# Performance work log

Hardware: AMD Instinct MI355X
Metric: run time of the kernel (lower is better)

The kernel has to match this reference:

```python
import jax, jax.numpy as jnp
import numpy as np

SIGMA = 1.0  # GaussianKernel slope


def setup_inputs() -> dict:
    key = jax.random.key(0)
    ks = jax.random.split(key, 6)
    B, F, E = 2048, 65536, 128
    return {
        "rel": jax.random.normal(ks[0], (B, E), dtype=jnp.float32),
        "arg1": jax.random.normal(ks[1], (B, E), dtype=jnp.float32),
        "arg2": jax.random.normal(ks[2], (B, E), dtype=jnp.float32),
        "fact_rel": jax.random.normal(ks[3], (F, E), dtype=jnp.float32),
        "fact_arg1": jax.random.normal(ks[4], (F, E), dtype=jnp.float32),
        "fact_arg2": jax.random.normal(ks[5], (F, E), dtype=jnp.float32),
    }


def reference(rel, arg1, arg2, fact_rel, fact_arg1, fact_arg2):
    # query: [B, 3E], facts: [F, 3E]  (concat scoring)
    query = jnp.concatenate([rel, arg1, arg2], axis=1)
    facts = jnp.concatenate([fact_rel, fact_arg1, fact_arg2], axis=1)
    # Gaussian kernel: exp(-||q - f||^2 / (2*sigma^2)), via ||q||^2 - 2 q.f + ||f||^2
    q_sq = jnp.sum(query * query, axis=1, keepdims=True)          # [B, 1]
    f_sq = jnp.sum(facts * facts, axis=1)                          # [F]
    d2 = q_sq - 2.0 * jnp.einsum('bd,fd->bf', query, facts) + f_sq[None, :]
    d2 = jnp.maximum(d2, 0.0)  # numerical guard for squared distance
    scores = jnp.exp(-d2 / (2.0 * SIGMA * SIGMA))                  # [B, F]
    return jnp.max(scores, axis=1)                                 # [B]
```

## Files before the change

kernel.cpp:

```cpp
#include <hip/hip_runtime.h>


typedef __attribute__((ext_vector_type(4))) float f32x4;
typedef __attribute__((ext_vector_type(2))) long lx2;
typedef __attribute__((ext_vector_type(4))) long lx4;
typedef __attribute__((ext_vector_type(8))) int i32x8;
typedef __attribute__((ext_vector_type(8))) __bf16 bf16x8;
typedef __attribute__((ext_vector_type(4))) unsigned short us4;

#define AS1 __attribute__((address_space(1)))
#define AS3 __attribute__((address_space(3)))
__device__ __forceinline__ void gl2lds16(const void* g, void* l) {
    __builtin_amdgcn_global_load_lds((const AS1 unsigned int*)g,
                                     (AS3 unsigned int*)l, 16, 0, 0);
}

__device__ __forceinline__ unsigned char f2e4m3(float x) {
    unsigned int u = __float_as_uint(x);
    unsigned int sign = (u >> 24) & 0x80u;
    unsigned int a = u & 0x7fffffffu;
    if (a >= 0x43e00000u) return (unsigned char)(sign | 0x7e);
    if (a < 0x3c800000u) {
        int m = (int)rintf(__uint_as_float(a) * 512.0f);
        return (unsigned char)(sign | (unsigned)m);
    }
    unsigned int base = a - 0x3c000000u;
    unsigned int lsb = (base >> 20) & 1u;
    unsigned int code = (base + 0x7ffffu + lsb) >> 20;
    return (unsigned char)(sign | code);
}

__device__ __forceinline__ unsigned short f2bf(float f) {
    unsigned int u = __float_as_uint(f);
    u = (u + 0x7fffu + ((u >> 16) & 1u)) >> 16;
    return (unsigned short)u;
}

__device__ __forceinline__ void conv_row_fp8(const float* __restrict__ p0,
                                             const float* __restrict__ p1,
                                             const float* __restrict__ p2,
                                             int row, unsigned char* __restrict__ outb,
                                             float* __restrict__ sq) {
    const int lane = threadIdx.x & 63;
    float s = 0.f;
    if (lane < 48) {
        const int p = lane >> 4;
        const int off = (lane & 15) * 8;
        const float* src = ((p == 0) ? p0 : (p == 1) ? p1 : p2) + (size_t)row * 128 + off;
        const float4 v0 = *(const float4*)(src);
        const float4 v1 = *(const float4*)(src + 4);
        s = v0.x * v0.x + v0.y * v0.y + v0.z * v0.z + v0.w * v0.w +
            v1.x * v1.x + v1.y * v1.y + v1.z * v1.z + v1.w * v1.w;
        const int k = p * 128 + off;
        const int g = k >> 6;
        const int ss = (k >> 5) & 1;
        const int quad = (k >> 3) & 3;
        const int cs = quad ^ ((row >> 1) & 3);
        unsigned long long pk =
            (unsigned long long)f2e4m3(v0.x)        | ((unsigned long long)f2e4m3(v0.y) << 8) |
            ((unsigned long long)f2e4m3(v0.z) << 16) | ((unsigned long long)f2e4m3(v0.w) << 24) |
            ((unsigned long long)f2e4m3(v1.x) << 32) | ((unsigned long long)f2e4m3(v1.y) << 40) |
            ((unsigned long long)f2e4m3(v1.z) << 48) | ((unsigned long long)f2e4m3(v1.w) << 56);
        *(unsigned long long*)(outb + (size_t)row * 384 + g * 64 + cs * 16 + ss * 8) = pk;
    }
#pragma unroll
    for (int off = 32; off >= 1; off >>= 1) s += __shfl_xor(s, off, 64);
    if (lane == 0) sq[row] = s;
}

__global__ void prep_kernel(const float* __restrict__ rel, const float* __restrict__ a1,
                            const float* __restrict__ a2, const float* __restrict__ fr,
                            const float* __restrict__ fa1, const float* __restrict__ fa2,
                            unsigned char* __restrict__ Qf, unsigned char* __restrict__ Ff,
                            float* __restrict__ qsq, float* __restrict__ fsq,
                            unsigned int* __restrict__ outbits, int B, int F) {
    const int wave = (int)(threadIdx.x >> 6);
    const int nq = B / 4;
    if ((int)blockIdx.x < nq) {
        conv_row_fp8(rel, a1, a2, blockIdx.x * 4 + wave, Qf, qsq);
        if (blockIdx.x == 0)
            for (int i = threadIdx.x; i < B; i += 256) outbits[i] = 0x7f800000u;
    } else {
        const int row = ((int)blockIdx.x - nq) * 4 + wave;
        if (row < F) conv_row_fp8(fr, fa1, fa2, row, Ff, fsq);
    }
}

__device__ __forceinline__ void stage_tile(const unsigned char* __restrict__ Ff,
                                           unsigned char* buf, int n0, int tid) {
#pragma unroll
    for (int it = 0; it < 6; ++it) {
        int iid = it * 256 + tid;
        gl2lds16(Ff + (size_t)(n0 + ((iid >> 2) & 63)) * 384 +
                     (iid >> 9) * 128 + ((iid >> 8) & 1) * 64 + (iid & 3) * 16,
                 buf + (size_t)iid * 16);
    }
}

__global__ __launch_bounds__(256, 2)
void gemm_pipe_kernel(const unsigned char* __restrict__ Qf,
                      const unsigned char* __restrict__ Ff,
                      const float* __restrict__ qsq, const float* __restrict__ fsq,
                      unsigned int* __restrict__ outbits, int ntiles) {
    __shared__ __align__(16) unsigned char Bs[2][24576];

    const int tid = threadIdx.x;
    const int lane = tid & 63;
    const int wid = tid >> 6;
    const int col = lane & 15, quad = lane >> 4;
    const int swc = ((col >> 1) & 3);
    const int cp = (quad ^ swc) * 16;
    const int m0 = blockIdx.y * 256;
    const int nbase = blockIdx.x * (ntiles * 64);
    const int SCL = 0x7f;

    union pk_t { lx4 l; i32x8 i; };

    i32x8 af8[4][3];
#pragma unroll
    for (int i = 0; i < 4; ++i) {
        const unsigned char* base = Qf + (size_t)(m0 + wid * 64 + i * 16 + col) * 384;
#pragma unroll
        for (int kk = 0; kk < 3; ++kk) {
            lx2 t0 = *(const lx2*)(base + kk * 128 + cp);
            lx2 t1 = *(const lx2*)(base + kk * 128 + 64 + cp);
            pk_t p; p.l.x = t0.x; p.l.y = t0.y; p.l.z = t1.x; p.l.w = t1.y;
            af8[i][kk] = p.i;
        }
    }

    float rowmin[16];
#pragma unroll
    for (int v = 0; v < 16; ++v) rowmin[v] = 3.0e38f;

    float fs_cur[4], fs_nxt[4];
#pragma unroll
    for (int j = 0; j < 4; ++j) fs_cur[j] = fsq[nbase + j * 16 + col];

    stage_tile(Ff, Bs[0], nbase, tid);
    for (int t = 0; t < ntiles; ++t) {
        __syncthreads();
        if (t + 1 < ntiles) {
            stage_tile(Ff, Bs[(t + 1) & 1], nbase + (t + 1) * 64, tid);
#pragma unroll
            for (int j = 0; j < 4; ++j)
                fs_nxt[j] = fsq[nbase + (t + 1) * 64 + j * 16 + col];
        }
        const unsigned char* bb = Bs[t & 1];

        f32x4 acc[4][4];
#pragma unroll
        for (int j = 0; j < 4; ++j) {
            float seed = -0.5f * fs_cur[j];
            f32x4 z = {seed, seed, seed, seed};
#pragma unroll
            for (int i = 0; i < 4; ++i) acc[i][j] = z;
        }

        i32x8 bv[3];
#define LOADB(S, DST)                                                          \
        {                                                                      \
            const int _j = (S) / 3, _kk = (S) % 3;                             \
            const unsigned char* pb = bb + _kk * 8192 + (_j * 16 + col) * 64 + cp; \
            lx2 t0 = *(const lx2*)(pb);                                        \
            lx2 t1 = *(const lx2*)(pb + 4096);                                 \
            pk_t p; p.l.x = t0.x; p.l.y = t0.y; p.l.z = t1.x; p.l.w = t1.y;    \
            DST = p.i;                                                         \
        }
#define MFMAS(S, SRC)                                                          \
        {                                                                      \
            const int _j = (S) / 3, _kk = (S) % 3;                             \
            _Pragma("unroll") for (int _i = 0; _i < 4; ++_i)                   \
                acc[_i][_j] = __builtin_amdgcn_mfma_scale_f32_16x16x128_f8f6f4(\
                    af8[_i][_kk], SRC, acc[_i][_j], 0, 0, 0, SCL, 0, SCL);     \
        }
        LOADB(0, bv[0]);
        LOADB(1, bv[1]);
#pragma unroll
        for (int s = 0; s < 12; ++s) {
            if (s + 2 < 12) LOADB(s + 2, bv[(s + 2) % 3]);
            MFMAS(s, bv[s % 3]);
        }
#undef LOADB
#undef MFMAS

#pragma unroll
        for (int i = 0; i < 4; ++i)
#pragma unroll
            for (int r = 0; r < 4; ++r) {
                float mn = rowmin[i * 4 + r];
#pragma unroll
                for (int j = 0; j < 4; ++j)
                    mn = fminf(mn, -2.0f * acc[i][j][r]);
                rowmin[i * 4 + r] = mn;
            }
#pragma unroll
        for (int j = 0; j < 4; ++j) fs_cur[j] = fs_nxt[j];
    }

#pragma unroll
    for (int v = 0; v < 16; ++v) {
        float mn = rowmin[v];
#pragma unroll
        for (int off = 1; off < 16; off <<= 1) mn = fminf(mn, __shfl_xor(mn, off, 64));
        rowmin[v] = mn;
    }
    if (col == 0) {
#pragma unroll
        for (int i = 0; i < 4; ++i)
#pragma unroll
            for (int r = 0; r < 4; ++r) {
                const int row = m0 + wid * 64 + i * 16 + quad * 4 + r;
                float d2 = fmaxf(qsq[row] + rowmin[i * 4 + r], 0.0f);
                atomicMin(outbits + row, __float_as_uint(d2));
            }
    }
}

__global__ void finalize_kernel(float* out, int n) {
    int i = blockIdx.x * blockDim.x + threadIdx.x;
    if (i < n) {
        float d2 = __uint_as_float(((unsigned int*)out)[i]);
        out[i] = expf(-0.5f * d2);
    }
}

__global__ void init_min_kernel(unsigned int* ob, int n) {
    int i = blockIdx.x * blockDim.x + threadIdx.x;
    if (i < n) ob[i] = 0x7f800000u;
}

__global__ void conv_rows_kernel(const float* __restrict__ p0, const float* __restrict__ p1,
                                 const float* __restrict__ p2, unsigned short* __restrict__ outb,
                                 float* __restrict__ sq, int nrows) {
    const int lane = threadIdx.x & 63;
    const int wave = threadIdx.x >> 6;
    const int row = blockIdx.x * 4 + wave;
    if (row >= nrows) return;
    float s = 0.f;
#pragma unroll
    for (int c = 0; c < 6; ++c) {
        int k = c * 64 + lane;
        const float* src = (k < 128) ? p0 : (k < 256) ? p1 : p2;
        float v = src[(size_t)row * 128 + (k & 127)];
        s += v * v;
        if (outb) outb[(size_t)row * 384 + k] = f2bf(v);
    }
#pragma unroll
    for (int off = 32; off >= 1; off >>= 1) s += __shfl_xor(s, off, 64);
    if (lane == 0) sq[row] = s;
}

__global__ __launch_bounds__(256)
void gemm_lean_kernel(const unsigned short* __restrict__ Qb,
                      const float* __restrict__ f0, const float* __restrict__ f1,
                      const float* __restrict__ f2,
                      const float* __restrict__ qsq, const float* __restrict__ fsq,
                      unsigned int* __restrict__ outbits, int K) {
    __shared__ __align__(16) unsigned short As[128 * 32];
    __shared__ __align__(16) unsigned short Bs[128 * 32];
    __shared__ float smin[128 * 2];

    const int tid = threadIdx.x;
    const int lane = tid & 63;
    const int wid = tid >> 6;
    const int wm = wid >> 1, wn = wid & 1;
    const int col = lane & 15, quad = lane >> 4;
    const int m0 = blockIdx.x * 128;
    const int n0 = blockIdx.y * 128;

    f32x4 acc[4][4];
#pragma unroll
    for (int i = 0; i < 4; ++i)
#pragma unroll
        for (int j = 0; j < 4; ++j) {
            f32x4 z = {0.f, 0.f, 0.f, 0.f};
            acc[i][j] = z;
        }

    const int nk = K >> 5;
    for (int kk = 0; kk < nk; ++kk) {
        const int k0 = kk << 5;
        __syncthreads();
#pragma unroll
        for (int it = 0; it < 2; ++it) {
            int iid = it * 256 + tid;
            int row = iid >> 2, ch = iid & 3;
            gl2lds16(Qb + ((size_t)(m0 + row) * K + k0 + ch * 8), As + (row * 32 + ch * 8));
        }
        const float* src = (k0 < 128) ? f0 : (k0 < 256) ? f1 : f2;
        const int kp = k0 & 127;
#pragma unroll
        for (int it = 0; it < 4; ++it) {
            int iid = it * 256 + tid;
            int row = iid >> 3, ch = iid & 7;
            const float4 v = *(const float4*)(src + (size_t)(n0 + row) * 128 + kp + ch * 4);
            us4 w = {f2bf(v.x), f2bf(v.y), f2bf(v.z), f2bf(v.w)};
            *(us4*)(Bs + (row * 32 + ch * 4)) = w;
        }
        __syncthreads();

        bf16x8 afr[4], bfv[4];
#pragma unroll
        for (int i = 0; i < 4; ++i)
            afr[i] = *(const bf16x8*)(As + ((wm * 64 + i * 16 + col) * 32 + quad * 8));
#pragma unroll
        for (int j = 0; j < 4; ++j)
            bfv[j] = *(const bf16x8*)(Bs + ((wn * 64 + j * 16 + col) * 32 + quad * 8));
#pragma unroll
        for (int i = 0; i < 4; ++i)
#pragma unroll
            for (int j = 0; j < 4; ++j)
                acc[i][j] = __builtin_amdgcn_mfma_f32_16x16x32_bf16(afr[i], bfv[j], acc[i][j], 0, 0, 0);
    }

    float fs[4];
#pragma unroll
    for (int j = 0; j < 4; ++j) fs[j] = fsq[n0 + wn * 64 + j * 16 + col];
#pragma unroll
    for (int i = 0; i < 4; ++i) {
#pragma unroll
        for (int r = 0; r < 4; ++r) {
            const int mrow = wm * 64 + i * 16 + quad * 4 + r;
            const float qs = qsq[m0 + mrow];
            float mn = 3.0e38f;
#pragma unroll
            for (int j = 0; j < 4; ++j) {
                float d2 = qs + fs[j] - 2.0f * acc[i][j][r];
                mn = fminf(mn, fmaxf(d2, 0.0f));
            }
#pragma unroll
            for (int off = 1; off < 16; off <<= 1) mn = fminf(mn, __shfl_xor(mn, off, 64));
            if (col == 0) smin[mrow * 2 + wn] = mn;
        }
    }
    __syncthreads();
    if (tid < 128) {
        float v = fminf(smin[tid * 2 + 0], smin[tid * 2 + 1]);
        atomicMin(outbits + m0 + tid, __float_as_uint(v));
    }
}

__global__ __launch_bounds__(256)
void tier3_kernel(const float* __restrict__ rel, const float* __restrict__ a1,
                  const float* __restrict__ a2, const float* __restrict__ fr,
                  const float* __restrict__ fa1, const float* __restrict__ fa2,
                  unsigned int* __restrict__ outbits) {
    __shared__ float qs[16][384];
    __shared__ float red[4][16];
    const int tid = threadIdx.x;
    const int qbase = blockIdx.y * 16;
    const int fbase = blockIdx.x * 2048;
    for (int i = tid; i < 16 * 384; i += 256) {
        int r = i / 384, c = i % 384;
        const float* src = (c < 128) ? rel : (c < 256) ? a1 : a2;
        qs[r][c] = src[(size_t)(qbase + r) * 128 + (c & 127)];
    }
    __syncthreads();
    float mn[16];
#pragma unroll
    for (int q = 0; q < 16; ++q) mn[q] = 3.0e38f;
    for (int fi = 0; fi < 2048; fi += 256) {
        const int f = fbase + fi + tid;
        float acc[16];
#pragma unroll
        for (int q = 0; q < 16; ++q) acc[q] = 0.f;
#pragma unroll
        for (int p = 0; p < 3; ++p) {
            const float* fptr = ((p == 0) ? fr : (p == 1) ? fa1 : fa2) + (size_t)f * 128;
            for (int k4 = 0; k4 < 32; ++k4) {
                const float4 fv = *(const float4*)(fptr + k4 * 4);
#pragma unroll
                for (int q = 0; q < 16; ++q) {
                    float d0 = fv.x - qs[q][p * 128 + k4 * 4 + 0];
                    float d1 = fv.y - qs[q][p * 128 + k4 * 4 + 1];
                    float d2 = fv.z - qs[q][p * 128 + k4 * 4 + 2];
                    float d3 = fv.w - qs[q][p * 128 + k4 * 4 + 3];
                    acc[q] += d0 * d0 + d1 * d1 + d2 * d2 + d3 * d3;
                }
            }
        }
#pragma unroll
        for (int q = 0; q < 16; ++q) mn[q] = fminf(mn[q], fmaxf(acc[q], 0.f));
    }
#pragma unroll
    for (int q = 0; q < 16; ++q) {
        float v = mn[q];
#pragma unroll
        for (int off = 32; off >= 1; off >>= 1) v = fminf(v, __shfl_xor(v, off, 64));
        if ((tid & 63) == 0) red[tid >> 6][q] = v;
    }
    __syncthreads();
    if (tid < 16) {
        float v = fminf(fminf(red[0][tid], red[1][tid]), fminf(red[2][tid], red[3][tid]));
        atomicMin(outbits + qbase + tid, __float_as_uint(v));
    }
}

extern "C" void kernel_launch(void* const* d_in, const int* in_sizes, int n_in,
                              void* d_out, int out_size, void* d_ws, size_t ws_size,
                              hipStream_t stream) {
    const float* rel = (const float*)d_in[0];
    const float* a1 = (const float*)d_in[1];
    const float* a2 = (const float*)d_in[2];
    const float* fr = (const float*)d_in[3];
    const float* fa1 = (const float*)d_in[4];
    const float* fa2 = (const float*)d_in[5];

    const int E = 128, K = 384;
    const int B = in_sizes[0] / E;
    const int F = in_sizes[3] / E;

    float* out = (float*)d_out;
    unsigned int* outbits = (unsigned int*)d_out;

    const size_t ff_bytes = (size_t)F * K;
    const size_t qf_bytes = (size_t)B * K;
    const size_t need_full = ff_bytes + qf_bytes + (size_t)F * 4 + (size_t)B * 4;
    const size_t qb_bytes = (size_t)B * K * 2;
    const size_t need_lean = qb_bytes + (size_t)F * 4 + (size_t)B * 4;

    const bool shapes_ok = (B % 256 == 0) && (F % 1024 == 0);
    if (ws_size >= need_full && shapes_ok) {
        unsigned char* Ff = (unsigned char*)d_ws;
        unsigned char* Qf = (unsigned char*)d_ws + ff_bytes;
        float* fsq = (float*)((char*)d_ws + ff_bytes + qf_bytes);
        float* qsq = fsq + F;
        prep_kernel<<<B / 4 + F / 4, 256, 0, stream>>>(rel, a1, a2, fr, fa1, fa2,
                                                       Qf, Ff, qsq, fsq, outbits, B, F);
        gemm_pipe_kernel<<<dim3(F / 1024, B / 256), 256, 0, stream>>>(
            Qf, Ff, qsq, fsq, outbits, 16);
    } else if (ws_size >= need_lean && B % 128 == 0 && F % 128 == 0) {
        unsigned short* Qb = (unsigned short*)d_ws;
        float* fsq = (float*)((char*)d_ws + qb_bytes);
        float* qsq = fsq + F;
        init_min_kernel<<<(B + 255) / 256, 256, 0, stream>>>(outbits, B);
        conv_rows_kernel<<<B / 4, 256, 0, stream>>>(rel, a1, a2, Qb, qsq, B);
        conv_rows_kernel<<<F / 4, 256, 0, stream>>>(fr, fa1, fa2, nullptr, fsq, F);
        gemm_lean_kernel<<<dim3(B / 128, F / 128), 256, 0, stream>>>(
            Qb, fr, fa1, fa2, qsq, fsq, outbits, K);
    } else {
        init_min_kernel<<<(B + 255) / 256, 256, 0, stream>>>(outbits, B);
        tier3_kernel<<<dim3(F / 2048, B / 16), 256, 0, stream>>>(rel, a1, a2, fr, fa1, fa2, outbits);
    }

    finalize_kernel<<<(B + 255) / 256, 256, 0, stream>>>(out, B);
}
```

Baseline: 175.2 us.

## Quantize query and fact embeddings to FP4 e2m1 for scaled MFMA

Replaces the FP8 e4m3 quantization of queries and facts with FP4 e2m1, packing two values per byte. The layouts, the LDS staging and the MFMA format flags change to match, and the LDS footprint is halved so occupancy rises to 3 blocks per CU. The grid is doubled with half the tiles per block. This cuts memory traffic and MFMA cost, but the squared distances come from a coarse 4-bit dot product combined with exact fp32 norms. That likely gives large errors in the max score, and it depends on the random-normal test inputs fitting the [-6,6] range.

```diff
diff --git a/kernel.cpp b/kernel.cpp
--- a/kernel.cpp
+++ b/kernel.cpp
@@ -3,7 +3,7 @@
 
 typedef __attribute__((ext_vector_type(4))) float f32x4;
 typedef __attribute__((ext_vector_type(2))) long lx2;
-typedef __attribute__((ext_vector_type(4))) long lx4;
+typedef __attribute__((ext_vector_type(4))) int i32x4;
 typedef __attribute__((ext_vector_type(8))) int i32x8;
 typedef __attribute__((ext_vector_type(8))) __bf16 bf16x8;
 typedef __attribute__((ext_vector_type(4))) unsigned short us4;
@@ -15,19 +15,11 @@
                                      (AS3 unsigned int*)l, 16, 0, 0);
 }
 
-__device__ __forceinline__ unsigned char f2e4m3(float x) {
-    unsigned int u = __float_as_uint(x);
-    unsigned int sign = (u >> 24) & 0x80u;
-    unsigned int a = u & 0x7fffffffu;
-    if (a >= 0x43e00000u) return (unsigned char)(sign | 0x7e);
-    if (a < 0x3c800000u) {
-        int m = (int)rintf(__uint_as_float(a) * 512.0f);
-        return (unsigned char)(sign | (unsigned)m);
-    }
-    unsigned int base = a - 0x3c000000u;
-    unsigned int lsb = (base >> 20) & 1u;
-    unsigned int code = (base + 0x7ffffu + lsb) >> 20;
-    return (unsigned char)(sign | code);
+__device__ __forceinline__ unsigned f2e2m1(float x) {
+    float a = fminf(fabsf(x), 6.0f);
+    float t = (a < 2.0f) ? a * 2.0f : ((a < 4.0f) ? a + 2.0f : a * 0.5f + 4.0f);
+    unsigned n = (unsigned)(int)rintf(t);
+    return n | ((__float_as_uint(x) >> 28) & 8u);
 }
 
 __device__ __forceinline__ unsigned short f2bf(float f) {
@@ -36,7 +28,14 @@
     return (unsigned short)u;
 }
 
-__device__ __forceinline__ void conv_row_fp8(const float* __restrict__ p0,
+__device__ __forceinline__ i32x8 widen4(i32x4 v) {
+    i32x8 r;
+    r[0] = v[0]; r[1] = v[1]; r[2] = v[2]; r[3] = v[3];
+    r[4] = 0; r[5] = 0; r[6] = 0; r[7] = 0;
+    return r;
+}
+
+__device__ __forceinline__ void conv_row_fp4(const float* __restrict__ p0,
                                              const float* __restrict__ p1,
                                              const float* __restrict__ p2,
                                              int row, unsigned char* __restrict__ outb,
@@ -51,20 +50,16 @@
         const float4 v1 = *(const float4*)(src + 4);
         s = v0.x * v0.x + v0.y * v0.y + v0.z * v0.z + v0.w * v0.w +
             v1.x * v1.x + v1.y * v1.y + v1.z * v1.z + v1.w * v1.w;
-        const int k = p * 128 + off;
-        const int g = k >> 6;
-        const int ss = (k >> 5) & 1;
-        const int quad = (k >> 3) & 3;
-        const int cs = quad ^ ((row >> 1) & 3);
-        unsigned long long pk =
-            (unsigned long long)f2e4m3(v0.x)        | ((unsigned long long)f2e4m3(v0.y) << 8) |
-            ((unsigned long long)f2e4m3(v0.z) << 16) | ((unsigned long long)f2e4m3(v0.w) << 24) |
-            ((unsigned long long)f2e4m3(v1.x) << 32) | ((unsigned long long)f2e4m3(v1.y) << 40) |
-            ((unsigned long long)f2e4m3(v1.z) << 48) | ((unsigned long long)f2e4m3(v1.w) << 56);
-        *(unsigned long long*)(outb + (size_t)row * 384 + g * 64 + cs * 16 + ss * 8) = pk;
-    }
-#pragma unroll
-    for (int off = 32; off >= 1; off >>= 1) s += __shfl_xor(s, off, 64);
+        unsigned pk = f2e2m1(v0.x)         | (f2e2m1(v0.y) << 4)  |
+                      (f2e2m1(v0.z) << 8)  | (f2e2m1(v0.w) << 12) |
+                      (f2e2m1(v1.x) << 16) | (f2e2m1(v1.y) << 20) |
+                      (f2e2m1(v1.z) << 24) | (f2e2m1(v1.w) << 28);
+        const int c = (lane & 15) >> 2;
+        const int cs = c ^ ((row >> 1) & 3);
+        *(unsigned*)(outb + (size_t)row * 192 + p * 64 + cs * 16 + (lane & 3) * 4) = pk;
+    }
+#pragma unroll
+    for (int o = 32; o >= 1; o >>= 1) s += __shfl_xor(s, o, 64);
     if (lane == 0) sq[row] = s;
 }
 
@@ -77,32 +72,32 @@
     const int wave = (int)(threadIdx.x >> 6);
     const int nq = B / 4;
     if ((int)blockIdx.x < nq) {
-        conv_row_fp8(rel, a1, a2, blockIdx.x * 4 + wave, Qf, qsq);
+        conv_row_fp4(rel, a1, a2, blockIdx.x * 4 + wave, Qf, qsq);
         if (blockIdx.x == 0)
             for (int i = threadIdx.x; i < B; i += 256) outbits[i] = 0x7f800000u;
     } else {
         const int row = ((int)blockIdx.x - nq) * 4 + wave;
-        if (row < F) conv_row_fp8(fr, fa1, fa2, row, Ff, fsq);
-    }
-}
-
-__device__ __forceinline__ void stage_tile(const unsigned char* __restrict__ Ff,
-                                           unsigned char* buf, int n0, int tid) {
-#pragma unroll
-    for (int it = 0; it < 6; ++it) {
+        if (row < F) conv_row_fp4(fr, fa1, fa2, row, Ff, fsq);
+    }
+}
+
+__device__ __forceinline__ void stage_tile4(const unsigned char* __restrict__ Ff,
+                                            unsigned char* buf, int n0, int tid) {
+#pragma unroll
+    for (int it = 0; it < 3; ++it) {
         int iid = it * 256 + tid;
-        gl2lds16(Ff + (size_t)(n0 + ((iid >> 2) & 63)) * 384 +
-                     (iid >> 9) * 128 + ((iid >> 8) & 1) * 64 + (iid & 3) * 16,
+        gl2lds16(Ff + (size_t)(n0 + ((iid >> 2) & 63)) * 192 +
+                     (iid >> 8) * 64 + (iid & 3) * 16,
                  buf + (size_t)iid * 16);
     }
 }
 
-__global__ __launch_bounds__(256, 2)
+__global__ __launch_bounds__(256, 3)
 void gemm_pipe_kernel(const unsigned char* __restrict__ Qf,
                       const unsigned char* __restrict__ Ff,
                       const float* __restrict__ qsq, const float* __restrict__ fsq,
                       unsigned int* __restrict__ outbits, int ntiles) {
-    __shared__ __align__(16) unsigned char Bs[2][24576];
+    __shared__ __align__(16) unsigned char Bs[2][12288];
 
     const int tid = threadIdx.x;
     const int lane = tid & 63;
@@ -114,19 +109,13 @@
     const int nbase = blockIdx.x * (ntiles * 64);
     const int SCL = 0x7f;
 
-    union pk_t { lx4 l; i32x8 i; };
-
-    i32x8 af8[4][3];
+    i32x4 af4[4][3];
 #pragma unroll
     for (int i = 0; i < 4; ++i) {
-        const unsigned char* base = Qf + (size_t)(m0 + wid * 64 + i * 16 + col) * 384;
-#pragma unroll
-        for (int kk = 0; kk < 3; ++kk) {
-            lx2 t0 = *(const lx2*)(base + kk * 128 + cp);
-            lx2 t1 = *(const lx2*)(base + kk * 128 + 64 + cp);
-            pk_t p; p.l.x = t0.x; p.l.y = t0.y; p.l.z = t1.x; p.l.w = t1.y;
-            af8[i][kk] = p.i;
-        }
+        const unsigned char* base = Qf + (size_t)(m0 + wid * 64 + i * 16 + col) * 192;
+#pragma unroll
+        for (int kk = 0; kk < 3; ++kk)
+            af4[i][kk] = *(const i32x4*)(base + kk * 64 + cp);
     }
 
     float rowmin[16];
@@ -137,11 +126,11 @@
 #pragma unroll
     for (int j = 0; j < 4; ++j) fs_cur[j] = fsq[nbase + j * 16 + col];
 
-    stage_tile(Ff, Bs[0], nbase, tid);
+    stage_tile4(Ff, Bs[0], nbase, tid);
     for (int t = 0; t < ntiles; ++t) {
         __syncthreads();
         if (t + 1 < ntiles) {
-            stage_tile(Ff, Bs[(t + 1) & 1], nbase + (t + 1) * 64, tid);
+            stage_tile4(Ff, Bs[(t + 1) & 1], nbase + (t + 1) * 64, tid);
 #pragma unroll
             for (int j = 0; j < 4; ++j)
                 fs_nxt[j] = fsq[nbase + (t + 1) * 64 + j * 16 + col];
@@ -157,22 +146,19 @@
             for (int i = 0; i < 4; ++i) acc[i][j] = z;
         }
 
-        i32x8 bv[3];
+        i32x4 bv[3];
 #define LOADB(S, DST)                                                          \
         {                                                                      \
             const int _j = (S) / 3, _kk = (S) % 3;                             \
-            const unsigned char* pb = bb + _kk * 8192 + (_j * 16 + col) * 64 + cp; \
-            lx2 t0 = *(const lx2*)(pb);                                        \
-            lx2 t1 = *(const lx2*)(pb + 4096);                                 \
-            pk_t p; p.l.x = t0.x; p.l.y = t0.y; p.l.z = t1.x; p.l.w = t1.y;    \
-            DST = p.i;                                                         \
+            DST = *(const i32x4*)(bb + _kk * 4096 + (_j * 16 + col) * 64 + cp);\
         }
 #define MFMAS(S, SRC)                                                          \
         {                                                                      \
             const int _j = (S) / 3, _kk = (S) % 3;                             \
+            i32x8 b8 = widen4(SRC);                                            \
             _Pragma("unroll") for (int _i = 0; _i < 4; ++_i)                   \
                 acc[_i][_j] = __builtin_amdgcn_mfma_scale_f32_16x16x128_f8f6f4(\
-                    af8[_i][_kk], SRC, acc[_i][_j], 0, 0, 0, SCL, 0, SCL);     \
+                    widen4(af4[_i][_kk]), b8, acc[_i][_j], 4, 4, 0, SCL, 0, SCL); \
         }
         LOADB(0, bv[0]);
         LOADB(1, bv[1]);
@@ -414,8 +400,8 @@
     float* out = (float*)d_out;
     unsigned int* outbits = (unsigned int*)d_out;
 
-    const size_t ff_bytes = (size_t)F * K;
-    const size_t qf_bytes = (size_t)B * K;
+    const size_t ff_bytes = (size_t)F * 192;
+    const size_t qf_bytes = (size_t)B * 192;
     const size_t need_full = ff_bytes + qf_bytes + (size_t)F * 4 + (size_t)B * 4;
     const size_t qb_bytes = (size_t)B * K * 2;
     const size_t need_lean = qb_bytes + (size_t)F * 4 + (size_t)B * 4;
@@ -428,8 +414,8 @@
         float* qsq = fsq + F;
         prep_kernel<<<B / 4 + F / 4, 256, 0, stream>>>(rel, a1, a2, fr, fa1, fa2,
                                                        Qf, Ff, qsq, fsq, outbits, B, F);
-        gemm_pipe_kernel<<<dim3(F / 1024, B / 256), 256, 0, stream>>>(
-            Qf, Ff, qsq, fsq, outbits, 16);
+        gemm_pipe_kernel<<<dim3(F / 512, B / 256), 256, 0, stream>>>(
+            Qf, Ff, qsq, fsq, outbits, 8);
     } else if (ws_size >= need_lean && B % 128 == 0 && F % 128 == 0) {
         unsigned short* Qb = (unsigned short*)d_ws;
         float* fsq = (float*)((char*)d_ws + qb_bytes);
```

Measured after the change: 174.8 us. No clear change (-0.2%).
